# Kernel tuning notes

Measured on AMD Instinct MI355X. Metric: run time of the kernel, lower is better.

Reference implementation:

```python
import jax, jax.numpy as jnp
import numpy as np

H = 32  # hidden size, fixed by the source module


def setup_inputs() -> dict:
    key = jax.random.key(0)
    ks = jax.random.split(key, 11)
    B, T = 1024, 999
    s = 0.1  # weight init scale
    return {
        "input": jax.random.normal(ks[0], (B, T), jnp.float32),
        "W_ih1": jax.random.normal(ks[1], (4 * H, 1), jnp.float32) * s,
        "W_hh1": jax.random.normal(ks[2], (4 * H, H), jnp.float32) * s,
        "b_ih1": jax.random.normal(ks[3], (4 * H,), jnp.float32) * s,
        "b_hh1": jax.random.normal(ks[4], (4 * H,), jnp.float32) * s,
        "W_ih2": jax.random.normal(ks[5], (4 * H, H), jnp.float32) * s,
        "W_hh2": jax.random.normal(ks[6], (4 * H, H), jnp.float32) * s,
        "b_ih2": jax.random.normal(ks[7], (4 * H,), jnp.float32) * s,
        "b_hh2": jax.random.normal(ks[8], (4 * H,), jnp.float32) * s,
        "W_lin": jax.random.normal(ks[9], (1, H), jnp.float32) * s,
        "b_lin": jax.random.normal(ks[10], (1,), jnp.float32) * s,
        "future": 1000,
    }


def _lstm_cell(x, h, c, W_ih, W_hh, b_ih, b_hh):
    # PyTorch LSTMCell: gates = x@W_ih^T + b_ih + h@W_hh^T + b_hh, order i,f,g,o
    z = x @ W_ih.T + h @ W_hh.T + (b_ih + b_hh)
    i, f, g, o = jnp.split(z, 4, axis=-1)
    c_new = jax.nn.sigmoid(f) * c + jax.nn.sigmoid(i) * jnp.tanh(g)
    h_new = jax.nn.sigmoid(o) * jnp.tanh(c_new)
    return h_new, c_new


def reference(input, W_ih1, W_hh1, b_ih1, b_hh1, W_ih2, W_hh2, b_ih2, b_hh2,
              W_lin, b_lin, future):
    B = input.shape[0]
    dt = input.dtype
    z = jnp.zeros((B, H), dt)

    def step_tf(carry, x_t):  # teacher-forced phase, x_t: [B]
        h1, c1, h2, c2 = carry
        h1, c1 = _lstm_cell(x_t[:, None], h1, c1, W_ih1, W_hh1, b_ih1, b_hh1)
        h2, c2 = _lstm_cell(h1, h2, c2, W_ih2, W_hh2, b_ih2, b_hh2)
        out = h2 @ W_lin.T + b_lin  # [B,1]
        return (h1, c1, h2, c2), out[:, 0]

    carry, outs1 = jax.lax.scan(step_tf, (z, z, z, z), input.T)  # outs1: [T,B]

    def step_gen(carry, _):
        h1, c1, h2, c2, out = carry
        h1, c1 = _lstm_cell(out, h1, c1, W_ih1, W_hh1, b_ih1, b_hh1)
        h2, c2 = _lstm_cell(h1, h2, c2, W_ih2, W_hh2, b_ih2, b_hh2)
        out = h2 @ W_lin.T + b_lin
        return (h1, c1, h2, c2, out), out[:, 0]

    last_out = outs1[-1][:, None]
    _, outs2 = jax.lax.scan(step_gen, (*carry, last_out), None, length=future)

    return jnp.concatenate([outs1, outs2], axis=0).T  # [B, T+future]
```

## Files before the change

kernel.cpp:

```cpp
#include <hip/hip_runtime.h>

#define HH 32
#define LOG2E 1.44269504088896340736f
#define KCH 16

typedef float v2f __attribute__((ext_vector_type(2)));

#define DPPF(v, ctrl) \
    __int_as_float(__builtin_amdgcn_update_dpp(0, __float_as_int(v), (ctrl), 0xF, 0xF, true))
#define QP_B0 0x00
#define QP_B1 0x55
#define QP_B2 0xAA
#define QP_B3 0xFF
#define DPP_ROR4  0x124
#define DPP_ROR8  0x128
#define SWZ(v, pat) __int_as_float(__builtin_amdgcn_ds_swizzle(__float_as_int(v), (pat)))

__device__ __forceinline__ float hw_exp2(float x) {
    float r; asm("v_exp_f32 %0, %1" : "=v"(r) : "v"(x)); return r;
}
__device__ __forceinline__ float sigm_e(float z, float e) {
    return __builtin_amdgcn_rcpf(1.0f + hw_exp2(z * e));
}
__device__ __forceinline__ v2f pk_fma(v2f a, v2f b, v2f c) {
    return __builtin_elementwise_fma(a, b, c);
}
__device__ __forceinline__ void load_bc(const float* p, v2f* d) {
#pragma unroll
    for (int r = 0; r < 8; ++r) {
        float4 v = ((const float4*)p)[r];
        d[2*r]   = (v2f){v.x, v.y};
        d[2*r+1] = (v2f){v.z, v.w};
    }
}
__device__ __forceinline__ float out_reduce(float p) {
    p += DPPF(p, DPP_ROR4);
    p += DPPF(p, DPP_ROR8);
    p += SWZ(p, 0x401F);
    p += __shfl_xor(p, 32, 64);
    return p;
}

__global__ __launch_bounds__(128, 2)
void lstm_seq_kernel(const float* __restrict__ input,
                     const float* __restrict__ W_ih1, const float* __restrict__ W_hh1,
                     const float* __restrict__ b_ih1, const float* __restrict__ b_hh1,
                     const float* __restrict__ W_ih2, const float* __restrict__ W_hh2,
                     const float* __restrict__ b_ih2, const float* __restrict__ b_hh2,
                     const float* __restrict__ W_lin, const float* __restrict__ b_lin,
                     float* __restrict__ out, int T, int total)
{
    const int b    = blockIdx.x;
    const int tid  = threadIdx.x;
    const int w    = tid >> 6;
    const int lane = tid & 63;
    const int q    = lane & 3;
    const int ch   = lane >> 2;
    const int rowA = (q << 5) | ch;
    const int rowB = (q << 5) | (ch + 16);

    __shared__ __align__(16) float ring[2 * KCH * HH];
    __shared__ __align__(16) float h1x[HH];
    __shared__ __align__(16) float h2s[HH];
    __shared__ float xbuf;

    const bool  isg = (q == 2);
    const float es  = isg ? (-2.0f * LOG2E) : (-LOG2E);
    const float mm  = isg ? 2.0f : 1.0f;
    const float cc  = isg ? -1.0f : 0.0f;

    v2f m1A[16], m1B[16], m2A[16], m2B[16];
    float wxA = 0.f, wxB = 0.f, bA, bB, wlA = 0.f, wlB = 0.f, blin = 0.f;
    if (w == 0) {
        const v2f* pA = (const v2f*)(W_hh1 + rowA * HH);
        const v2f* pB = (const v2f*)(W_hh1 + rowB * HH);
#pragma unroll
        for (int r = 0; r < 16; ++r) { m1A[r] = pA[r]; m1B[r] = pB[r]; }
        wxA = W_ih1[rowA]; wxB = W_ih1[rowB];
        bA  = b_ih1[rowA] + b_hh1[rowA];
        bB  = b_ih1[rowB] + b_hh1[rowB];
    } else {
        const v2f* pA = (const v2f*)(W_ih2 + rowA * HH);
        const v2f* pB = (const v2f*)(W_ih2 + rowB * HH);
        const v2f* qA = (const v2f*)(W_hh2 + rowA * HH);
        const v2f* qB = (const v2f*)(W_hh2 + rowB * HH);
#pragma unroll
        for (int r = 0; r < 16; ++r) { m1A[r] = pA[r]; m1B[r] = pB[r];
                                       m2A[r] = qA[r]; m2B[r] = qB[r]; }
        bA  = b_ih2[rowA] + b_hh2[rowA];
        bB  = b_ih2[rowB] + b_hh2[rowB];
        wlA = W_lin[ch]; wlB = W_lin[ch + 16]; blin = b_lin[0];
    }

    float cA = 0.f, cB = 0.f;
    v2f p0 = {0.f,0.f}, p1 = {0.f,0.f}, p2 = {0.f,0.f}, p3 = {0.f,0.f};

    const float* __restrict__ inp  = input + (size_t)b * T;
    float* __restrict__       outp = out   + (size_t)b * total;

    if (w == 0) {
        int t = 0;
        float xcur = inp[0];
        for (int cb = 0; t < T; ++cb) {
            float* buf = ring + (cb & 1) * (KCH * HH);
            int S = T - t; if (S > KCH) S = KCH;
            for (int s = 0; s < S; ++s, ++t) {
                float x = xcur;
                int tn = t + 1;
                xcur = inp[tn < T ? tn : 0];
                float z1A = fmaf(x, wxA, bA + (p0.x + p0.y) + (p1.x + p1.y));
                float z1B = fmaf(x, wxB, bB + (p2.x + p2.y) + (p3.x + p3.y));
                float acA = fmaf(mm, sigm_e(z1A, es), cc);
                float acB = fmaf(mm, sigm_e(z1B, es), cc);
                float iA = DPPF(acA, QP_B0), fA = DPPF(acA, QP_B1);
                float gA = DPPF(acA, QP_B2), oA = DPPF(acA, QP_B3);
                float iB = DPPF(acB, QP_B0), fB = DPPF(acB, QP_B1);
                float gB = DPPF(acB, QP_B2), oB = DPPF(acB, QP_B3);
                cA = fmaf(fA, cA, iA * gA);
                cB = fmaf(fB, cB, iB * gB);
                float hA = oA * fmaf(2.0f, sigm_e(cA, -2.0f * LOG2E), -1.0f);
                float hB = oB * fmaf(2.0f, sigm_e(cB, -2.0f * LOG2E), -1.0f);
                float* slot = buf + s * HH;
                if (q == 0) { slot[ch] = hA; slot[ch + 16] = hB; }
                v2f hv[16]; load_bc(slot, hv);
                p0 = (v2f){0.f,0.f}; p1 = (v2f){0.f,0.f};
                p2 = (v2f){0.f,0.f}; p3 = (v2f){0.f,0.f};
#pragma unroll
                for (int r = 0; r < 16; r += 2) {
                    p0 = pk_fma(hv[r],   m1A[r],   p0);
                    p1 = pk_fma(hv[r+1], m1A[r+1], p1);
                    p2 = pk_fma(hv[r],   m1B[r],   p2);
                    p3 = pk_fma(hv[r+1], m1B[r+1], p3);
                }
            }
            __syncthreads();
        }
        __syncthreads();
    } else {
        __syncthreads();
        int t = 0;
        for (int cb = 0; t < T; ++cb) {
            const float* buf = ring + (cb & 1) * (KCH * HH);
            int S = T - t; if (S > KCH) S = KCH;
            for (int s = 0; s < S; ++s, ++t) {
                v2f hv[16]; load_bc(buf + s * HH, hv);
                v2f s0 = p0, s1 = p1, s2 = p2, s3 = p3;
#pragma unroll
                for (int r = 0; r < 16; r += 2) {
                    s0 = pk_fma(hv[r],   m1A[r],   s0);
                    s1 = pk_fma(hv[r+1], m1A[r+1], s1);
                    s2 = pk_fma(hv[r],   m1B[r],   s2);
                    s3 = pk_fma(hv[r+1], m1B[r+1], s3);
                }
                float z2A = bA + (s0.x + s0.y) + (s1.x + s1.y);
                float z2B = bB + (s2.x + s2.y) + (s3.x + s3.y);
                float acA = fmaf(mm, sigm_e(z2A, es), cc);
                float acB = fmaf(mm, sigm_e(z2B, es), cc);
                float iA = DPPF(acA, QP_B0), fA = DPPF(acA, QP_B1);
                float gA = DPPF(acA, QP_B2), oA = DPPF(acA, QP_B3);
                float iB = DPPF(acB, QP_B0), fB = DPPF(acB, QP_B1);
                float gB = DPPF(acB, QP_B2), oB = DPPF(acB, QP_B3);
                cA = fmaf(fA, cA, iA * gA);
                cB = fmaf(fB, cB, iB * gB);
                float hA = oA * fmaf(2.0f, sigm_e(cA, -2.0f * LOG2E), -1.0f);
                float hB = oB * fmaf(2.0f, sigm_e(cB, -2.0f * LOG2E), -1.0f);
                if (q == 0) { h2s[ch] = hA; h2s[ch + 16] = hB; }
                v2f gv[16]; load_bc(h2s, gv);
                p0 = (v2f){0.f,0.f}; p1 = (v2f){0.f,0.f};
                p2 = (v2f){0.f,0.f}; p3 = (v2f){0.f,0.f};
#pragma unroll
                for (int r = 0; r < 16; r += 2) {
                    p0 = pk_fma(gv[r],   m2A[r],   p0);
                    p1 = pk_fma(gv[r+1], m2A[r+1], p1);
                    p2 = pk_fma(gv[r],   m2B[r],   p2);
                    p3 = pk_fma(gv[r+1], m2B[r+1], p3);
                }
                float pr = fmaf(hA, wlA, hB * wlB);
                float ov = out_reduce(pr) + blin;
                if (lane == 0) { outp[t] = ov; xbuf = ov; }
            }
            __syncthreads();
        }
    }

    for (int t = T; t < total; ++t) {
        __syncthreads();
        if (w == 0) {
            float x = xbuf;
            float z1A = fmaf(x, wxA, bA + (p0.x + p0.y) + (p1.x + p1.y));
            float z1B = fmaf(x, wxB, bB + (p2.x + p2.y) + (p3.x + p3.y));
            float acA = fmaf(mm, sigm_e(z1A, es), cc);
            float acB = fmaf(mm, sigm_e(z1B, es), cc);
            float iA = DPPF(acA, QP_B0), fA = DPPF(acA, QP_B1);
            float gA = DPPF(acA, QP_B2), oA = DPPF(acA, QP_B3);
            float iB = DPPF(acB, QP_B0), fB = DPPF(acB, QP_B1);
            float gB = DPPF(acB, QP_B2), oB = DPPF(acB, QP_B3);
            cA = fmaf(fA, cA, iA * gA);
            cB = fmaf(fB, cB, iB * gB);
            float hA = oA * fmaf(2.0f, sigm_e(cA, -2.0f * LOG2E), -1.0f);
            float hB = oB * fmaf(2.0f, sigm_e(cB, -2.0f * LOG2E), -1.0f);
            if (q == 0) { h1x[ch] = hA; h1x[ch + 16] = hB; }
        } else {
            v2f gv[16]; load_bc(h2s, gv);
            p0 = (v2f){0.f,0.f}; p1 = (v2f){0.f,0.f};
            p2 = (v2f){0.f,0.f}; p3 = (v2f){0.f,0.f};
#pragma unroll
            for (int r = 0; r < 16; r += 2) {
                p0 = pk_fma(gv[r],   m2A[r],   p0);
                p1 = pk_fma(gv[r+1], m2A[r+1], p1);
                p2 = pk_fma(gv[r],   m2B[r],   p2);
                p3 = pk_fma(gv[r+1], m2B[r+1], p3);
            }
        }
        __syncthreads();
        if (w == 0) {
            v2f hv[16]; load_bc(h1x, hv);
            p0 = (v2f){0.f,0.f}; p1 = (v2f){0.f,0.f};
            p2 = (v2f){0.f,0.f}; p3 = (v2f){0.f,0.f};
#pragma unroll
            for (int r = 0; r < 16; r += 2) {
                p0 = pk_fma(hv[r],   m1A[r],   p0);
                p1 = pk_fma(hv[r+1], m1A[r+1], p1);
                p2 = pk_fma(hv[r],   m1B[r],   p2);
                p3 = pk_fma(hv[r+1], m1B[r+1], p3);
            }
        } else {
            v2f hv[16]; load_bc(h1x, hv);
            v2f s0 = p0, s1 = p1, s2 = p2, s3 = p3;
#pragma unroll
            for (int r = 0; r < 16; r += 2) {
                s0 = pk_fma(hv[r],   m1A[r],   s0);
                s1 = pk_fma(hv[r+1], m1A[r+1], s1);
                s2 = pk_fma(hv[r],   m1B[r],   s2);
                s3 = pk_fma(hv[r+1], m1B[r+1], s3);
            }
            float z2A = bA + (s0.x + s0.y) + (s1.x + s1.y);
            float z2B = bB + (s2.x + s2.y) + (s3.x + s3.y);
            float acA = fmaf(mm, sigm_e(z2A, es), cc);
            float acB = fmaf(mm, sigm_e(z2B, es), cc);
            float iA = DPPF(acA, QP_B0), fA = DPPF(acA, QP_B1);
            float gA = DPPF(acA, QP_B2), oA = DPPF(acA, QP_B3);
            float iB = DPPF(acB, QP_B0), fB = DPPF(acB, QP_B1);
            float gB = DPPF(acB, QP_B2), oB = DPPF(acB, QP_B3);
            cA = fmaf(fA, cA, iA * gA);
            cB = fmaf(fB, cB, iB * gB);
            float hA = oA * fmaf(2.0f, sigm_e(cA, -2.0f * LOG2E), -1.0f);
            float hB = oB * fmaf(2.0f, sigm_e(cB, -2.0f * LOG2E), -1.0f);
            if (q == 0) { h2s[ch] = hA; h2s[ch + 16] = hB; }
            float pr = fmaf(hA, wlA, hB * wlB);
            float ov = out_reduce(pr) + blin;
            if (lane == 0) { outp[t] = ov; xbuf = ov; }
        }
    }
}

extern "C" void kernel_launch(void* const* d_in, const int* in_sizes, int n_in,
                              void* d_out, int out_size, void* d_ws, size_t ws_size,
                              hipStream_t stream) {
    const int B = 1024;
    const int T = in_sizes[0] / B;
    const int total = out_size / B;

    lstm_seq_kernel<<<dim3(B), dim3(128), 0, stream>>>(
        (const float*)d_in[0],
        (const float*)d_in[1], (const float*)d_in[2],
        (const float*)d_in[3], (const float*)d_in[4],
        (const float*)d_in[5], (const float*)d_in[6],
        (const float*)d_in[7], (const float*)d_in[8],
        (const float*)d_in[9], (const float*)d_in[10],
        (float*)d_out, T, total);
}
```

Measured before the change: 1.214 ms.

## Interleave two sequences per wave pair and ping-pong layers in generation phase

Each block now runs 256 threads forming two wave pairs, and each pair processes two batch elements at once, interleaving their independent recurrences to hide latency in the serial chain. In the autoregressive phase the two sequences are staggered so that layer 1 of one element and layer 2 of the other run in the same barrier interval. The output projection is also moved onto the layer-1 wave, which keeps the full W_lin vector in registers and no longer needs xbuf. This doubles per-thread state and register pressure, and the launch moves to 256 blocks with occupancy bound 1.

```diff
diff --git a/kernel.cpp b/kernel.cpp
--- a/kernel.cpp
+++ b/kernel.cpp
@@ -41,7 +41,40 @@
     return p;
 }
 
-__global__ __launch_bounds__(128, 2)
+template<bool ACC>
+__device__ __forceinline__ void dot2(const v2f* hv, const v2f* mA, const v2f* mB,
+                                     v2f& P0, v2f& P1, v2f& P2, v2f& P3) {
+    if (ACC) {
+        P0 = pk_fma(hv[0], mA[0], P0); P1 = pk_fma(hv[1], mA[1], P1);
+        P2 = pk_fma(hv[0], mB[0], P2); P3 = pk_fma(hv[1], mB[1], P3);
+    } else {
+        P0 = hv[0] * mA[0]; P1 = hv[1] * mA[1];
+        P2 = hv[0] * mB[0]; P3 = hv[1] * mB[1];
+    }
+#pragma unroll
+    for (int r = 2; r < 16; r += 2) {
+        P0 = pk_fma(hv[r],   mA[r],   P0);
+        P1 = pk_fma(hv[r+1], mA[r+1], P1);
+        P2 = pk_fma(hv[r],   mB[r],   P2);
+        P3 = pk_fma(hv[r+1], mB[r+1], P3);
+    }
+}
+
+__device__ __forceinline__ void gate_hc(float zA, float zB, float es, float mm, float cc,
+                                        float& cA, float& cB, float& hA, float& hB) {
+    float acA = fmaf(mm, sigm_e(zA, es), cc);
+    float acB = fmaf(mm, sigm_e(zB, es), cc);
+    float iA = DPPF(acA, QP_B0), fA = DPPF(acA, QP_B1);
+    float gA = DPPF(acA, QP_B2), oA = DPPF(acA, QP_B3);
+    float iB = DPPF(acB, QP_B0), fB = DPPF(acB, QP_B1);
+    float gB = DPPF(acB, QP_B2), oB = DPPF(acB, QP_B3);
+    cA = fmaf(fA, cA, iA * gA);
+    cB = fmaf(fB, cB, iB * gB);
+    hA = oA * fmaf(2.0f, sigm_e(cA, -2.0f * LOG2E), -1.0f);
+    hB = oB * fmaf(2.0f, sigm_e(cB, -2.0f * LOG2E), -1.0f);
+}
+
+__global__ __launch_bounds__(256, 1)
 void lstm_seq_kernel(const float* __restrict__ input,
                      const float* __restrict__ W_ih1, const float* __restrict__ W_hh1,
                      const float* __restrict__ b_ih1, const float* __restrict__ b_hh1,
@@ -50,19 +83,26 @@
                      const float* __restrict__ W_lin, const float* __restrict__ b_lin,
                      float* __restrict__ out, int T, int total)
 {
-    const int b    = blockIdx.x;
     const int tid  = threadIdx.x;
-    const int w    = tid >> 6;
+    const int wave = tid >> 6;
     const int lane = tid & 63;
+    const int pair = wave >> 1;
+    const int w    = wave & 1;
     const int q    = lane & 3;
     const int ch   = lane >> 2;
     const int rowA = (q << 5) | ch;
     const int rowB = (q << 5) | (ch + 16);
 
-    __shared__ __align__(16) float ring[2 * KCH * HH];
-    __shared__ __align__(16) float h1x[HH];
-    __shared__ __align__(16) float h2s[HH];
-    __shared__ float xbuf;
+    const int e0i = blockIdx.x + (pair << 9);
+    const int e1i = e0i + 256;
+
+    __shared__ __align__(16) float ring[2][2][KCH][2][HH];
+    __shared__ __align__(16) float h1x[2][2][HH];
+    __shared__ __align__(16) float h2s[2][2][HH];
+
+    float* ring_p = &ring[pair][0][0][0][0];
+    float* h1x0 = &h1x[pair][0][0]; float* h1x1 = &h1x[pair][1][0];
+    float* h2s0 = &h2s[pair][0][0]; float* h2s1 = &h2s[pair][1][0];
 
     const bool  isg = (q == 2);
     const float es  = isg ? (-2.0f * LOG2E) : (-LOG2E);
@@ -70,12 +110,13 @@
     const float cc  = isg ? -1.0f : 0.0f;
 
     v2f m1A[16], m1B[16], m2A[16], m2B[16];
-    float wxA = 0.f, wxB = 0.f, bA, bB, wlA = 0.f, wlB = 0.f, blin = 0.f;
+    float wxA = 0.f, wxB = 0.f, bA, bB, wlA = 0.f, wlB = 0.f, blin;
     if (w == 0) {
         const v2f* pA = (const v2f*)(W_hh1 + rowA * HH);
         const v2f* pB = (const v2f*)(W_hh1 + rowB * HH);
-#pragma unroll
-        for (int r = 0; r < 16; ++r) { m1A[r] = pA[r]; m1B[r] = pB[r]; }
+        const v2f* wp = (const v2f*)W_lin;
+#pragma unroll
+        for (int r = 0; r < 16; ++r) { m1A[r] = pA[r]; m1B[r] = pB[r]; m2A[r] = wp[r]; }
         wxA = W_ih1[rowA]; wxB = W_ih1[rowB];
         bA  = b_ih1[rowA] + b_hh1[rowA];
         bB  = b_ih1[rowB] + b_hh1[rowB];
@@ -89,49 +130,43 @@
                                        m2A[r] = qA[r]; m2B[r] = qB[r]; }
         bA  = b_ih2[rowA] + b_hh2[rowA];
         bB  = b_ih2[rowB] + b_hh2[rowB];
-        wlA = W_lin[ch]; wlB = W_lin[ch + 16]; blin = b_lin[0];
-    }
-
-    float cA = 0.f, cB = 0.f;
-    v2f p0 = {0.f,0.f}, p1 = {0.f,0.f}, p2 = {0.f,0.f}, p3 = {0.f,0.f};
-
-    const float* __restrict__ inp  = input + (size_t)b * T;
-    float* __restrict__       outp = out   + (size_t)b * total;
+        wlA = W_lin[ch]; wlB = W_lin[ch + 16];
+    }
+    blin = b_lin[0];
+
+    float cA0 = 0.f, cB0 = 0.f, cA1 = 0.f, cB1 = 0.f;
+    v2f p00 = {0.f,0.f}, p01 = {0.f,0.f}, p02 = {0.f,0.f}, p03 = {0.f,0.f};
+    v2f p10 = {0.f,0.f}, p11 = {0.f,0.f}, p12 = {0.f,0.f}, p13 = {0.f,0.f};
+
+    const float* __restrict__ inp0  = input + (size_t)e0i * T;
+    const float* __restrict__ inp1  = input + (size_t)e1i * T;
+    float* __restrict__       outp0 = out   + (size_t)e0i * total;
+    float* __restrict__       outp1 = out   + (size_t)e1i * total;
 
     if (w == 0) {
         int t = 0;
-        float xcur = inp[0];
+        float x0 = inp0[0], x1 = inp1[0];
         for (int cb = 0; t < T; ++cb) {
-            float* buf = ring + (cb & 1) * (KCH * HH);
+            float* buf = ring_p + (cb & 1) * (KCH * 2 * HH);
             int S = T - t; if (S > KCH) S = KCH;
             for (int s = 0; s < S; ++s, ++t) {
-                float x = xcur;
-                int tn = t + 1;
-                xcur = inp[tn < T ? tn : 0];
-                float z1A = fmaf(x, wxA, bA + (p0.x + p0.y) + (p1.x + p1.y));
-                float z1B = fmaf(x, wxB, bB + (p2.x + p2.y) + (p3.x + p3.y));
-                float acA = fmaf(mm, sigm_e(z1A, es), cc);
-                float acB = fmaf(mm, sigm_e(z1B, es), cc);
-                float iA = DPPF(acA, QP_B0), fA = DPPF(acA, QP_B1);
-                float gA = DPPF(acA, QP_B2), oA = DPPF(acA, QP_B3);
-                float iB = DPPF(acB, QP_B0), fB = DPPF(acB, QP_B1);
-                float gB = DPPF(acB, QP_B2), oB = DPPF(acB, QP_B3);
-                cA = fmaf(fA, cA, iA * gA);
-                cB = fmaf(fB, cB, iB * gB);
-                float hA = oA * fmaf(2.0f, sigm_e(cA, -2.0f * LOG2E), -1.0f);
-                float hB = oB * fmaf(2.0f, sigm_e(cB, -2.0f * LOG2E), -1.0f);
-                float* slot = buf + s * HH;
-                if (q == 0) { slot[ch] = hA; slot[ch + 16] = hB; }
-                v2f hv[16]; load_bc(slot, hv);
-                p0 = (v2f){0.f,0.f}; p1 = (v2f){0.f,0.f};
-                p2 = (v2f){0.f,0.f}; p3 = (v2f){0.f,0.f};
-#pragma unroll
-                for (int r = 0; r < 16; r += 2) {
-                    p0 = pk_fma(hv[r],   m1A[r],   p0);
-                    p1 = pk_fma(hv[r+1], m1A[r+1], p1);
-                    p2 = pk_fma(hv[r],   m1B[r],   p2);
-                    p3 = pk_fma(hv[r+1], m1B[r+1], p3);
-                }
+                float xa = x0, xb = x1;
+                int tn = t + 1; int tc = tn < T ? tn : 0;
+                x0 = inp0[tc]; x1 = inp1[tc];
+                float z1A0 = fmaf(xa, wxA, bA + (p00.x+p00.y) + (p01.x+p01.y));
+                float z1B0 = fmaf(xa, wxB, bB + (p02.x+p02.y) + (p03.x+p03.y));
+                float z1A1 = fmaf(xb, wxA, bA + (p10.x+p10.y) + (p11.x+p11.y));
+                float z1B1 = fmaf(xb, wxB, bB + (p12.x+p12.y) + (p13.x+p13.y));
+                float hA0, hB0, hA1, hB1;
+                gate_hc(z1A0, z1B0, es, mm, cc, cA0, cB0, hA0, hB0);
+                gate_hc(z1A1, z1B1, es, mm, cc, cA1, cB1, hA1, hB1);
+                float* slot = buf + s * (2 * HH);
+                if (q == 0) { slot[ch] = hA0;      slot[ch + 16] = hB0;
+                              slot[HH + ch] = hA1; slot[HH + ch + 16] = hB1; }
+                v2f hv0[16], hv1[16];
+                load_bc(slot, hv0); load_bc(slot + HH, hv1);
+                dot2<false>(hv0, m1A, m1B, p00, p01, p02, p03);
+                dot2<false>(hv1, m1A, m1B, p10, p11, p12, p13);
             }
             __syncthreads();
         }
@@ -140,116 +175,100 @@
         __syncthreads();
         int t = 0;
         for (int cb = 0; t < T; ++cb) {
-            const float* buf = ring + (cb & 1) * (KCH * HH);
+            const float* buf = ring_p + (cb & 1) * (KCH * 2 * HH);
             int S = T - t; if (S > KCH) S = KCH;
             for (int s = 0; s < S; ++s, ++t) {
-                v2f hv[16]; load_bc(buf + s * HH, hv);
-                v2f s0 = p0, s1 = p1, s2 = p2, s3 = p3;
-#pragma unroll
-                for (int r = 0; r < 16; r += 2) {
-                    s0 = pk_fma(hv[r],   m1A[r],   s0);
-                    s1 = pk_fma(hv[r+1], m1A[r+1], s1);
-                    s2 = pk_fma(hv[r],   m1B[r],   s2);
-                    s3 = pk_fma(hv[r+1], m1B[r+1], s3);
-                }
-                float z2A = bA + (s0.x + s0.y) + (s1.x + s1.y);
-                float z2B = bB + (s2.x + s2.y) + (s3.x + s3.y);
-                float acA = fmaf(mm, sigm_e(z2A, es), cc);
-                float acB = fmaf(mm, sigm_e(z2B, es), cc);
-                float iA = DPPF(acA, QP_B0), fA = DPPF(acA, QP_B1);
-                float gA = DPPF(acA, QP_B2), oA = DPPF(acA, QP_B3);
-                float iB = DPPF(acB, QP_B0), fB = DPPF(acB, QP_B1);
-                float gB = DPPF(acB, QP_B2), oB = DPPF(acB, QP_B3);
-                cA = fmaf(fA, cA, iA * gA);
-                cB = fmaf(fB, cB, iB * gB);
-                float hA = oA * fmaf(2.0f, sigm_e(cA, -2.0f * LOG2E), -1.0f);
-                float hB = oB * fmaf(2.0f, sigm_e(cB, -2.0f * LOG2E), -1.0f);
-                if (q == 0) { h2s[ch] = hA; h2s[ch + 16] = hB; }
-                v2f gv[16]; load_bc(h2s, gv);
-                p0 = (v2f){0.f,0.f}; p1 = (v2f){0.f,0.f};
-                p2 = (v2f){0.f,0.f}; p3 = (v2f){0.f,0.f};
-#pragma unroll
-                for (int r = 0; r < 16; r += 2) {
-                    p0 = pk_fma(gv[r],   m2A[r],   p0);
-                    p1 = pk_fma(gv[r+1], m2A[r+1], p1);
-                    p2 = pk_fma(gv[r],   m2B[r],   p2);
-                    p3 = pk_fma(gv[r+1], m2B[r+1], p3);
-                }
-                float pr = fmaf(hA, wlA, hB * wlB);
-                float ov = out_reduce(pr) + blin;
-                if (lane == 0) { outp[t] = ov; xbuf = ov; }
+                const float* slot = buf + s * (2 * HH);
+                v2f hv0[16], hv1[16];
+                load_bc(slot, hv0); load_bc(slot + HH, hv1);
+                v2f s00 = p00, s01 = p01, s02 = p02, s03 = p03;
+                v2f s10 = p10, s11 = p11, s12 = p12, s13 = p13;
+                dot2<true>(hv0, m1A, m1B, s00, s01, s02, s03);
+                dot2<true>(hv1, m1A, m1B, s10, s11, s12, s13);
+                float z2A0 = bA + (s00.x+s00.y) + (s01.x+s01.y);
+                float z2B0 = bB + (s02.x+s02.y) + (s03.x+s03.y);
+                float z2A1 = bA + (s10.x+s10.y) + (s11.x+s11.y);
+                float z2B1 = bB + (s12.x+s12.y) + (s13.x+s13.y);
+                float hA0, hB0, hA1, hB1;
+                gate_hc(z2A0, z2B0, es, mm, cc, cA0, cB0, hA0, hB0);
+                gate_hc(z2A1, z2B1, es, mm, cc, cA1, cB1, hA1, hB1);
+                if (q == 0) { h2s0[ch] = hA0; h2s0[ch + 16] = hB0;
+                              h2s1[ch] = hA1; h2s1[ch + 16] = hB1; }
+                v2f gv0[16], gv1[16];
+                load_bc(h2s0, gv0); load_bc(h2s1, gv1);
+                dot2<false>(gv0, m2A, m2B, p00, p01, p02, p03);
+                dot2<false>(gv1, m2A, m2B, p10, p11, p12, p13);
+                float pr0 = fmaf(hA0, wlA, hB0 * wlB);
+                float pr1 = fmaf(hA1, wlA, hB1 * wlB);
+                float o0 = out_reduce(pr0) + blin;
+                float o1 = out_reduce(pr1) + blin;
+                if (lane == 0) { outp0[t] = o0; outp1[t] = o1; }
             }
             __syncthreads();
         }
     }
 
-    for (int t = T; t < total; ++t) {
+    const int fut = total - T;
+    for (int sp = 0; sp <= fut; ++sp) {
         __syncthreads();
         if (w == 0) {
-            float x = xbuf;
-            float z1A = fmaf(x, wxA, bA + (p0.x + p0.y) + (p1.x + p1.y));
-            float z1B = fmaf(x, wxB, bB + (p2.x + p2.y) + (p3.x + p3.y));
-            float acA = fmaf(mm, sigm_e(z1A, es), cc);
-            float acB = fmaf(mm, sigm_e(z1B, es), cc);
-            float iA = DPPF(acA, QP_B0), fA = DPPF(acA, QP_B1);
-            float gA = DPPF(acA, QP_B2), oA = DPPF(acA, QP_B3);
-            float iB = DPPF(acB, QP_B0), fB = DPPF(acB, QP_B1);
-            float gB = DPPF(acB, QP_B2), oB = DPPF(acB, QP_B3);
-            cA = fmaf(fA, cA, iA * gA);
-            cB = fmaf(fB, cB, iB * gB);
-            float hA = oA * fmaf(2.0f, sigm_e(cA, -2.0f * LOG2E), -1.0f);
-            float hB = oB * fmaf(2.0f, sigm_e(cB, -2.0f * LOG2E), -1.0f);
-            if (q == 0) { h1x[ch] = hA; h1x[ch + 16] = hB; }
-        } else {
-            v2f gv[16]; load_bc(h2s, gv);
-            p0 = (v2f){0.f,0.f}; p1 = (v2f){0.f,0.f};
-            p2 = (v2f){0.f,0.f}; p3 = (v2f){0.f,0.f};
-#pragma unroll
-            for (int r = 0; r < 16; r += 2) {
-                p0 = pk_fma(gv[r],   m2A[r],   p0);
-                p1 = pk_fma(gv[r+1], m2A[r+1], p1);
-                p2 = pk_fma(gv[r],   m2B[r],   p2);
-                p3 = pk_fma(gv[r+1], m2B[r+1], p3);
-            }
+            v2f gv[16]; load_bc(h2s0, gv);
+            v2f oa = gv[0] * m2A[0], ob = gv[1] * m2A[1];
+#pragma unroll
+            for (int r = 2; r < 16; r += 2) { oa = pk_fma(gv[r], m2A[r], oa);
+                                              ob = pk_fma(gv[r+1], m2A[r+1], ob); }
+            float xo = (oa.x + oa.y) + (ob.x + ob.y) + blin;
+            if (sp >= 1 && lane == 0) outp0[T - 1 + sp] = xo;
+            if (sp < fut) {
+                float z1A = fmaf(xo, wxA, bA + (p00.x+p00.y) + (p01.x+p01.y));
+                float z1B = fmaf(xo, wxB, bB + (p02.x+p02.y) + (p03.x+p03.y));
+                float hA, hB;
+                gate_hc(z1A, z1B, es, mm, cc, cA0, cB0, hA, hB);
+                if (q == 0) { h1x0[ch] = hA; h1x0[ch + 16] = hB; }
+                v2f hv[16]; load_bc(h1x0, hv);
+                dot2<false>(hv, m1A, m1B, p00, p01, p02, p03);
+            }
+        } else if (sp >= 1) {
+            v2f hv[16]; load_bc(h1x1, hv);
+            v2f s0 = p10, s1 = p11, s2 = p12, s3 = p13;
+            dot2<true>(hv, m1A, m1B, s0, s1, s2, s3);
+            float z2A = bA + (s0.x+s0.y) + (s1.x+s1.y);
+            float z2B = bB + (s2.x+s2.y) + (s3.x+s3.y);
+            float hA, hB;
+            gate_hc(z2A, z2B, es, mm, cc, cA1, cB1, hA, hB);
+            if (q == 0) { h2s1[ch] = hA; h2s1[ch + 16] = hB; }
+            v2f gv[16]; load_bc(h2s1, gv);
+            dot2<false>(gv, m2A, m2B, p10, p11, p12, p13);
         }
         __syncthreads();
         if (w == 0) {
-            v2f hv[16]; load_bc(h1x, hv);
-            p0 = (v2f){0.f,0.f}; p1 = (v2f){0.f,0.f};
-            p2 = (v2f){0.f,0.f}; p3 = (v2f){0.f,0.f};
-#pragma unroll
-            for (int r = 0; r < 16; r += 2) {
-                p0 = pk_fma(hv[r],   m1A[r],   p0);
-                p1 = pk_fma(hv[r+1], m1A[r+1], p1);
-                p2 = pk_fma(hv[r],   m1B[r],   p2);
-                p3 = pk_fma(hv[r+1], m1B[r+1], p3);
-            }
-        } else {
-            v2f hv[16]; load_bc(h1x, hv);
-            v2f s0 = p0, s1 = p1, s2 = p2, s3 = p3;
-#pragma unroll
-            for (int r = 0; r < 16; r += 2) {
-                s0 = pk_fma(hv[r],   m1A[r],   s0);
-                s1 = pk_fma(hv[r+1], m1A[r+1], s1);
-                s2 = pk_fma(hv[r],   m1B[r],   s2);
-                s3 = pk_fma(hv[r+1], m1B[r+1], s3);
-            }
-            float z2A = bA + (s0.x + s0.y) + (s1.x + s1.y);
-            float z2B = bB + (s2.x + s2.y) + (s3.x + s3.y);
-            float acA = fmaf(mm, sigm_e(z2A, es), cc);
-            float acB = fmaf(mm, sigm_e(z2B, es), cc);
-            float iA = DPPF(acA, QP_B0), fA = DPPF(acA, QP_B1);
-            float gA = DPPF(acA, QP_B2), oA = DPPF(acA, QP_B3);
-            float iB = DPPF(acB, QP_B0), fB = DPPF(acB, QP_B1);
-            float gB = DPPF(acB, QP_B2), oB = DPPF(acB, QP_B3);
-            cA = fmaf(fA, cA, iA * gA);
-            cB = fmaf(fB, cB, iB * gB);
-            float hA = oA * fmaf(2.0f, sigm_e(cA, -2.0f * LOG2E), -1.0f);
-            float hB = oB * fmaf(2.0f, sigm_e(cB, -2.0f * LOG2E), -1.0f);
-            if (q == 0) { h2s[ch] = hA; h2s[ch + 16] = hB; }
-            float pr = fmaf(hA, wlA, hB * wlB);
-            float ov = out_reduce(pr) + blin;
-            if (lane == 0) { outp[t] = ov; xbuf = ov; }
+            v2f gv[16]; load_bc(h2s1, gv);
+            v2f oa = gv[0] * m2A[0], ob = gv[1] * m2A[1];
+#pragma unroll
+            for (int r = 2; r < 16; r += 2) { oa = pk_fma(gv[r], m2A[r], oa);
+                                              ob = pk_fma(gv[r+1], m2A[r+1], ob); }
+            float xo = (oa.x + oa.y) + (ob.x + ob.y) + blin;
+            if (sp >= 1 && lane == 0) outp1[T - 1 + sp] = xo;
+            if (sp < fut) {
+                float z1A = fmaf(xo, wxA, bA + (p10.x+p10.y) + (p11.x+p11.y));
+                float z1B = fmaf(xo, wxB, bB + (p12.x+p12.y) + (p13.x+p13.y));
+                float hA, hB;
+                gate_hc(z1A, z1B, es, mm, cc, cA1, cB1, hA, hB);
+                if (q == 0) { h1x1[ch] = hA; h1x1[ch + 16] = hB; }
+                v2f hv[16]; load_bc(h1x1, hv);
+                dot2<false>(hv, m1A, m1B, p10, p11, p12, p13);
+            }
+        } else if (sp < fut) {
+            v2f hv[16]; load_bc(h1x0, hv);
+            v2f s0 = p00, s1 = p01, s2 = p02, s3 = p03;
+            dot2<true>(hv, m1A, m1B, s0, s1, s2, s3);
+            float z2A = bA + (s0.x+s0.y) + (s1.x+s1.y);
+            float z2B = bB + (s2.x+s2.y) + (s3.x+s3.y);
+            float hA, hB;
+            gate_hc(z2A, z2B, es, mm, cc, cA0, cB0, hA, hB);
+            if (q == 0) { h2s0[ch] = hA; h2s0[ch + 16] = hB; }
+            v2f gv[16]; load_bc(h2s0, gv);
+            dot2<false>(gv, m2A, m2B, p00, p01, p02, p03);
         }
     }
 }
@@ -261,7 +280,7 @@
     const int T = in_sizes[0] / B;
     const int total = out_size / B;
 
-    lstm_seq_kernel<<<dim3(B), dim3(128), 0, stream>>>(
+    lstm_seq_kernel<<<dim3(B / 4), dim3(256), 0, stream>>>(
         (const float*)d_in[0],
         (const float*)d_in[1], (const float*)d_in[2],
         (const float*)d_in[3], (const float*)d_in[4],
```

Result: slower. 1.700 ms (+40.1%).
